# Optimization experiments

Hardware: AMD Instinct MI355X
Metric: run time of the kernel (lower is better)

The kernel has to match this reference:

```python
import jax, jax.numpy as jnp
import numpy as np

NUM_NODES = 100000
NUM_EDGES = 1200000
IN_CH = 64
HID_CH = 64
NUM_REL = 8
DEG = NUM_EDGES // NUM_NODES  # uniform degree 12


def setup_inputs() -> dict:
    key = jax.random.key(0)
    k1, k2, k3, k4 = jax.random.split(key, 4)
    x = jax.random.normal(k1, (NUM_NODES, IN_CH), dtype=jnp.float32)
    linear = jax.random.normal(k2, (NUM_REL, IN_CH, HID_CH), dtype=jnp.float32) * (1.0 / np.sqrt(IN_CH))
    ptr = jnp.arange(NUM_NODES + 1, dtype=jnp.int64) * DEG  # CSR row pointers, uniform degree
    idx = jax.random.randint(k3, (NUM_EDGES,), 0, NUM_NODES, dtype=jnp.int64)
    edge_types = jax.random.randint(k4, (NUM_EDGES,), 0, NUM_REL, dtype=jnp.int64)
    return {"x": x, "linear": linear, "ptr": ptr, "idx": idx,
            "edge_types": edge_types, "num_node": NUM_NODES}


def reference(x, linear, ptr, idx, edge_types, num_node):
    # Gather source-node features per edge: [E, in]
    gathered = x[idx]
    # Per-edge-type linear transform (loop over small fixed num_rel, like RGCNOP)
    out_e = jnp.zeros((gathered.shape[0], linear.shape[-1]), dtype=gathered.dtype)
    for r in range(linear.shape[0]):
        mask = (edge_types == r).astype(gathered.dtype)[:, None]
        out_e = out_e + mask * (gathered @ linear[r])
    # CSR scatter-sum aggregation over destination segments defined by ptr
    num_edges = idx.shape[0]
    seg_ids = jnp.searchsorted(ptr, jnp.arange(num_edges, dtype=ptr.dtype), side='right') - 1
    agg = jax.ops.segment_sum(out_e, seg_ids, num_segments=num_node)
    # Degree normalization
    deg = (ptr[1:] - ptr[:-1]).astype(agg.dtype)
    return agg / deg[:, None]
```

## Files before the change

kernel.cpp:

```cpp
#include <hip/hip_runtime.h>
#include <hip/hip_bf16.h>
#include <hip/hip_fp16.h>


#define THREADS 512
#define NPB 32
#define KDIM 512
#define LDA 520
#define MAXE 512
#define WFRAG (4 * 16 * 64 * 8)

typedef __attribute__((ext_vector_type(8))) short bf16x8;
typedef __attribute__((ext_vector_type(4))) float f32x4;
typedef __attribute__((ext_vector_type(8))) unsigned short u16x8;

extern __shared__ __align__(16) char smem[];

__device__ __forceinline__ unsigned short f2bf(float f) {
  __hip_bfloat16 h = __float2bfloat16(f);
  return *reinterpret_cast<unsigned short*>(&h);
}

__device__ __forceinline__ float h2f(unsigned short u) {
  __half h;
  *reinterpret_cast<unsigned short*>(&h) = u;
  return __half2float(h);
}

__global__ __launch_bounds__(256) void pack_w(const void* __restrict__ wv,
                                              unsigned short* __restrict__ wsB) {
  const int lane = threadIdx.x & 63;
  const unsigned word = ((const unsigned*)wv)[lane];
  const int exf = (int)((word >> 7) & 0xFFu);
  const bool w_bf16 = __popcll(__ballot(exf >= 96 && exf < 160)) >= 48;
  for (int i = blockIdx.x * 256 + threadIdx.x; i < WFRAG; i += gridDim.x * 256) {
    const int j  = i & 7;
    const int l  = (i >> 3) & 63;
    const int kt = (i >> 9) & 15;
    const int nt = i >> 13;
    const int k  = kt * 32 + (l >> 4) * 8 + j;
    const int n  = nt * 16 + (l & 15);
    float v;
    if (w_bf16) v = __bfloat162float(((const __hip_bfloat16*)wv)[k * 64 + n]);
    else        v = ((const float*)wv)[k * 64 + n];
    wsB[i] = f2bf(v);
  }
}

__global__ __launch_bounds__(256) void pack_x(const void* __restrict__ xv,
                                              unsigned short* __restrict__ wsX,
                                              int total8) {
  const int lane = threadIdx.x & 63;
  const unsigned word = ((const unsigned*)xv)[lane];
  const int exf = (int)((word >> 7) & 0xFFu);
  const bool x_bf16 = __popcll(__ballot(exf >= 96 && exf < 160)) >= 48;
  if (x_bf16) return;
  const f32x4* xf = (const f32x4*)xv;
  for (int i = blockIdx.x * 256 + threadIdx.x; i < total8; i += gridDim.x * 256) {
    const f32x4 a = xf[i * 2 + 0];
    const f32x4 b = xf[i * 2 + 1];
    u16x8 o;
    __half h;
    h = __float2half(a[0]); o[0] = *reinterpret_cast<unsigned short*>(&h);
    h = __float2half(a[1]); o[1] = *reinterpret_cast<unsigned short*>(&h);
    h = __float2half(a[2]); o[2] = *reinterpret_cast<unsigned short*>(&h);
    h = __float2half(a[3]); o[3] = *reinterpret_cast<unsigned short*>(&h);
    h = __float2half(b[0]); o[4] = *reinterpret_cast<unsigned short*>(&h);
    h = __float2half(b[1]); o[5] = *reinterpret_cast<unsigned short*>(&h);
    h = __float2half(b[2]); o[6] = *reinterpret_cast<unsigned short*>(&h);
    h = __float2half(b[3]); o[7] = *reinterpret_cast<unsigned short*>(&h);
    ((u16x8*)wsX)[i] = o;
  }
}

#define ACC_SW(accrow, r, vv)                                        \
  switch (r) {                                                       \
    case 0: accrow[0] += (vv); break; case 1: accrow[1] += (vv); break; \
    case 2: accrow[2] += (vv); break; case 3: accrow[3] += (vv); break; \
    case 4: accrow[4] += (vv); break; case 5: accrow[5] += (vv); break; \
    case 6: accrow[6] += (vv); break; default: accrow[7] += (vv); break; }

__global__ __launch_bounds__(THREADS, 6)
void rgcn_fused(const void* __restrict__ xv,
                const void* __restrict__ wv,
                const int* __restrict__ p32,
                const int* __restrict__ i32,
                const int* __restrict__ t32,
                const unsigned short* __restrict__ wsB,
                const unsigned short* __restrict__ wsX,
                float* __restrict__ out,
                int num_nodes) {
  __hip_bfloat16* aggS = (__hip_bfloat16*)smem;
  __hip_bfloat16* wtS  = aggS + (NPB + 1) * LDA;
  char* tail = smem + (size_t)(NPB + 1) * LDA * 2 +
               (wsB ? 0 : (size_t)64 * LDA * 2);
  float*    invS  = (float*)tail;
  int*      ptrS  = (int*)(tail + 256);
  unsigned* eMeta = (unsigned*)(tail + 256 + 144);

  const int tid   = threadIdx.x;
  const int lane  = tid & 63;
  const int wvid  = tid >> 6;
  const int node0 = blockIdx.x * NPB;

  const unsigned xword = ((const unsigned*)xv)[lane];
  const int exf = (int)((xword >> 7) & 0xFFu);
  const bool x_bf16 = __popcll(__ballot(exf >= 96 && exf < 160)) >= 48;
  const bool idx64 = (p32[1] == 0);

  auto ldptr = [&](int n) -> int { return idx64 ? p32[2 * n] : p32[n]; };

  const int ntop   = min(node0 + NPB, num_nodes);
  const int e_lo   = ldptr(node0);
  const int ecount = ldptr(ntop) - e_lo;
  const bool staged = (ecount > 0 && ecount <= MAXE);

  for (int i = tid; i <= NPB; i += THREADS)
    ptrS[i] = ldptr(min(node0 + i, num_nodes));

  if (staged) {
    for (int e = tid; e < ecount; e += THREADS) {
      const int ge = e_lo + e;
      const unsigned s = (unsigned)(idx64 ? i32[2 * ge] : i32[ge]);
      const unsigned r = (unsigned)(idx64 ? t32[2 * ge] : t32[ge]);
      eMeta[e] = s | (r << 24);
    }
  }

  if (!wsB) {
    if (x_bf16) {
      const __hip_bfloat16* wb = (const __hip_bfloat16*)wv;
      for (int i = tid; i < KDIM * 64; i += THREADS)
        wtS[(i & 63) * LDA + (i >> 6)] = wb[i];
    } else {
      const float* wf = (const float*)wv;
      for (int i = tid; i < KDIM * 64; i += THREADS)
        wtS[(i & 63) * LDA + (i >> 6)] = __float2bfloat16(wf[i]);
    }
  }

  __syncthreads();

  for (int i = tid; i < NPB; i += THREADS) {
    const int d = ptrS[i + 1] - ptrS[i];
    invS[i] = (d > 0 && node0 + i < num_nodes) ? 1.0f / (float)d : 0.0f;
  }

  if (staged) {
    for (int n = tid; n < NPB; n += THREADS) {
      const int b0 = ptrS[n] - e_lo;
      const int d  = ptrS[n + 1] - ptrS[n];
      if (d == 12) {
        unsigned mm[12];
        unsigned long long cnt = 0;
#pragma unroll
        for (int i = 0; i < 12; ++i) {
          mm[i] = eMeta[b0 + i];
          cnt += 1ull << ((mm[i] >> 24) * 4);
        }
        unsigned long long off = 0;
        unsigned run = 0;
#pragma unroll
        for (int r = 0; r < 8; ++r) {
          off |= (unsigned long long)run << (r * 4);
          run += (unsigned)((cnt >> (r * 4)) & 15ull);
        }
#pragma unroll
        for (int i = 0; i < 12; ++i) {
          const int sh = (int)(mm[i] >> 24) * 4;
          const unsigned slot = (unsigned)((off >> sh) & 15ull);
          off += 1ull << sh;
          eMeta[b0 + (int)slot] = mm[i];
        }
      }
    }
  }

  {
    f32x4* z = (f32x4*)aggS;
    const f32x4 zero = {0.f, 0.f, 0.f, 0.f};
    const int nvec = (NPB + 1) * LDA * 2 / 16;
    for (int i = tid; i < nvec; i += THREADS) z[i] = zero;
  }

  __syncthreads();

  const int c16 = lane & 15;
  const int qd  = lane >> 4;

  auto gather = [&](auto xp, auto loadrow) {
    const int nlb = wvid * 4;
    const int eq0 = ptrS[nlb + qd] - e_lo;
    const int dq  = ptrS[nlb + qd + 1] - e_lo - eq0;
    const bool okfast = staged && (node0 + nlb + 3 < num_nodes) &&
                        (__ballot(dq == 12) == ~0ull);
    if (okfast) {
      unsigned m[12];
      unsigned rr[12];
#pragma unroll
      for (int j = 0; j < 12; ++j) m[j] = eMeta[eq0 + j];
#pragma unroll
      for (int j = 0; j < 12; ++j) rr[j] = m[j] >> 24;
      f32x4 v[12];
#pragma unroll
      for (int j = 0; j < 12; ++j)
        v[j] = loadrow((int)(m[j] & 0x00FFFFFFu), c16);
      unsigned short* nodeP =
          (unsigned short*)(aggS + (size_t)(nlb + qd) * LDA) + 4 * c16;
      unsigned short* dumpP =
          (unsigned short*)(aggS + (size_t)NPB * LDA) + qd * 136 + 4 * c16;
      f32x4 A = {0.f, 0.f, 0.f, 0.f};
#pragma unroll
      for (int j = 0; j < 12; ++j) {
        A += v[j];
        const bool b = (j == 11) || (rr[j] != rr[j + 1 < 12 ? j + 1 : 11]);
        ushort4 bb;
        bb.x = f2bf(A[0]); bb.y = f2bf(A[1]);
        bb.z = f2bf(A[2]); bb.w = f2bf(A[3]);
        unsigned short* dst = b ? (nodeP + (rr[j] << 6)) : dumpP;
        *(ushort4*)dst = bb;
        A = b ? (f32x4){0.f, 0.f, 0.f, 0.f} : A;
      }
    } else {
#pragma unroll
      for (int t = 0; t < 4; ++t) {
        const int nl = nlb + t;
        float a[8] = {0.f, 0.f, 0.f, 0.f, 0.f, 0.f, 0.f, 0.f};
        if (node0 + nl < num_nodes) {
          const int e0 = ptrS[nl] - e_lo, e1 = ptrS[nl + 1] - e_lo;
          for (int e = e0; e < e1; ++e) {
            unsigned mm;
            if (staged) mm = eMeta[e];
            else {
              const int ge = e_lo + e;
              mm = (unsigned)(idx64 ? i32[2 * ge] : i32[ge]) |
                   ((unsigned)(idx64 ? t32[2 * ge] : t32[ge]) << 24);
            }
            const float vv = xp((size_t)(mm & 0x00FFFFFFu) * 64 + lane);
            const int r = __builtin_amdgcn_readfirstlane((int)(mm >> 24));
            ACC_SW(a, r, vv)
          }
        }
#pragma unroll
        for (int r = 0; r < 8; ++r)
          aggS[(size_t)nl * LDA + r * 64 + lane] = __float2bfloat16(a[r]);
      }
    }
  };

  if (!x_bf16 && wsX) {
    auto xp = [&](size_t i) -> float { return h2f(wsX[i]); };
    auto lr = [&](int src, int c) -> f32x4 {
      const ushort4 u = ((const ushort4*)wsX)[(size_t)src * 16 + c];
      f32x4 f;
      f[0] = h2f(u.x); f[1] = h2f(u.y); f[2] = h2f(u.z); f[3] = h2f(u.w);
      return f;
    };
    gather(xp, lr);
  } else if (x_bf16) {
    auto xp = [&](size_t i) -> float {
      const unsigned short u = ((const unsigned short*)xv)[i];
      return __uint_as_float((unsigned)u << 16);
    };
    auto lr = [&](int src, int c) -> f32x4 {
      const ushort4 u = ((const ushort4*)xv)[(size_t)src * 16 + c];
      f32x4 f;
      f[0] = __uint_as_float((unsigned)(unsigned short)u.x << 16);
      f[1] = __uint_as_float((unsigned)(unsigned short)u.y << 16);
      f[2] = __uint_as_float((unsigned)(unsigned short)u.z << 16);
      f[3] = __uint_as_float((unsigned)(unsigned short)u.w << 16);
      return f;
    };
    gather(xp, lr);
  } else {
    auto xp = [&](size_t i) -> float { return ((const float*)xv)[i]; };
    auto lr = [&](int src, int c) -> f32x4 {
      return ((const f32x4*)xv)[(size_t)src * 16 + c];
    };
    gather(xp, lr);
  }

  __syncthreads();

  const int mt = wvid >> 2;
  const int nt = wvid & 3;
  const int mi = lane & 15;
  const int q4 = lane >> 4;
  const __hip_bfloat16* ap = aggS + (size_t)(mt * 16 + mi) * LDA + q4 * 8;
  f32x4 c0 = {0.f, 0.f, 0.f, 0.f};
  if (wsB) {
    const bf16x8* B = (const bf16x8*)wsB;
#pragma unroll
    for (int kt = 0; kt < KDIM / 32; ++kt) {
      const bf16x8 a = *(const bf16x8*)(ap + kt * 32);
      const bf16x8 b = B[(nt * 16 + kt) * 64 + lane];
      c0 = __builtin_amdgcn_mfma_f32_16x16x32_bf16(a, b, c0, 0, 0, 0);
    }
  } else {
    const __hip_bfloat16* bp = wtS + (size_t)(nt * 16 + mi) * LDA + q4 * 8;
#pragma unroll
    for (int kt = 0; kt < KDIM / 32; ++kt) {
      const bf16x8 a = *(const bf16x8*)(ap + kt * 32);
      const bf16x8 b = *(const bf16x8*)(bp + kt * 32);
      c0 = __builtin_amdgcn_mfma_f32_16x16x32_bf16(a, b, c0, 0, 0, 0);
    }
  }

#pragma unroll
  for (int i = 0; i < 4; ++i) {
    const int row  = q4 * 4 + i;
    const int nl   = mt * 16 + row;
    const int node = node0 + nl;
    if (node < num_nodes) {
      out[(size_t)node * 64 + nt * 16 + mi] = c0[i] * invS[nl];
    }
  }
}

extern "C" void kernel_launch(void* const* d_in, const int* in_sizes, int n_in,
                              void* d_out, int out_size, void* d_ws, size_t ws_size,
                              hipStream_t stream) {
  const void* x   = d_in[0];
  const void* w   = d_in[1];
  const int*  ptr = (const int*)d_in[2];
  const int*  idx = (const int*)d_in[3];
  const int*  et  = (const int*)d_in[4];
  float*      out = (float*)d_out;

  const int num_nodes = in_sizes[0] / 64;

  const size_t needW = (size_t)WFRAG * sizeof(unsigned short);
  const size_t needX = needW + (size_t)num_nodes * 64 * 2;
  const bool useWs = (d_ws != nullptr) && (ws_size >= needW);
  const bool useX  = (d_ws != nullptr) && (ws_size >= needX);
  unsigned short* wsB = useWs ? (unsigned short*)d_ws : nullptr;
  unsigned short* wsX = useX ? (unsigned short*)((char*)d_ws + needW) : nullptr;

  if (useWs) pack_w<<<32, 256, 0, stream>>>(w, wsB);
  if (useX)  pack_x<<<1024, 256, 0, stream>>>(x, wsX, num_nodes * 8);

  const size_t lds_bytes = (size_t)(NPB + 1) * LDA * 2 +
                           (useWs ? 0 : (size_t)64 * LDA * 2) +
                           256 + 144 + (size_t)MAXE * 4;

  hipFuncSetAttribute((const void*)rgcn_fused,
                      hipFuncAttributeMaxDynamicSharedMemorySize,
                      (int)lds_bytes);

  const int nblocks = (num_nodes + NPB - 1) / NPB;
  rgcn_fused<<<nblocks, THREADS, lds_bytes, stream>>>(x, w, ptr, idx, et, wsB,
                                                      wsX, out, num_nodes);
}
```

Measured before the change: 127.8 us.

## Merge pack kernels and prepack edge metadata into workspace

Combines the weight and x packing kernels into one launch that also packs each edge's source index and relation type into a single 32-bit word in the workspace. The main kernel then reads one word per edge instead of two int64 arrays, which cuts its index traffic. Output stores become nontemporal. In exchange the pre-pass must read and write all edge metadata every call, which adds a full extra pass over the index arrays.

```diff
diff --git a/kernel.cpp b/kernel.cpp
--- a/kernel.cpp
+++ b/kernel.cpp
@@ -27,49 +27,66 @@
   return __half2float(h);
 }
 
-__global__ __launch_bounds__(256) void pack_w(const void* __restrict__ wv,
-                                              unsigned short* __restrict__ wsB) {
+__global__ __launch_bounds__(256)
+void pack_all(const void* __restrict__ xv, const void* __restrict__ wv,
+              const int* __restrict__ p32, const int* __restrict__ i32,
+              const int* __restrict__ t32,
+              unsigned short* __restrict__ wsB,
+              unsigned* __restrict__ wsM,
+              unsigned short* __restrict__ wsX,
+              int num_nodes, int idx_words) {
   const int lane = threadIdx.x & 63;
-  const unsigned word = ((const unsigned*)wv)[lane];
-  const int exf = (int)((word >> 7) & 0xFFu);
-  const bool w_bf16 = __popcll(__ballot(exf >= 96 && exf < 160)) >= 48;
-  for (int i = blockIdx.x * 256 + threadIdx.x; i < WFRAG; i += gridDim.x * 256) {
-    const int j  = i & 7;
-    const int l  = (i >> 3) & 63;
-    const int kt = (i >> 9) & 15;
-    const int nt = i >> 13;
-    const int k  = kt * 32 + (l >> 4) * 8 + j;
-    const int n  = nt * 16 + (l & 15);
-    float v;
-    if (w_bf16) v = __bfloat162float(((const __hip_bfloat16*)wv)[k * 64 + n]);
-    else        v = ((const float*)wv)[k * 64 + n];
-    wsB[i] = f2bf(v);
-  }
-}
-
-__global__ __launch_bounds__(256) void pack_x(const void* __restrict__ xv,
-                                              unsigned short* __restrict__ wsX,
-                                              int total8) {
-  const int lane = threadIdx.x & 63;
-  const unsigned word = ((const unsigned*)xv)[lane];
-  const int exf = (int)((word >> 7) & 0xFFu);
-  const bool x_bf16 = __popcll(__ballot(exf >= 96 && exf < 160)) >= 48;
-  if (x_bf16) return;
-  const f32x4* xf = (const f32x4*)xv;
-  for (int i = blockIdx.x * 256 + threadIdx.x; i < total8; i += gridDim.x * 256) {
-    const f32x4 a = xf[i * 2 + 0];
-    const f32x4 b = xf[i * 2 + 1];
-    u16x8 o;
-    __half h;
-    h = __float2half(a[0]); o[0] = *reinterpret_cast<unsigned short*>(&h);
-    h = __float2half(a[1]); o[1] = *reinterpret_cast<unsigned short*>(&h);
-    h = __float2half(a[2]); o[2] = *reinterpret_cast<unsigned short*>(&h);
-    h = __float2half(a[3]); o[3] = *reinterpret_cast<unsigned short*>(&h);
-    h = __float2half(b[0]); o[4] = *reinterpret_cast<unsigned short*>(&h);
-    h = __float2half(b[1]); o[5] = *reinterpret_cast<unsigned short*>(&h);
-    h = __float2half(b[2]); o[6] = *reinterpret_cast<unsigned short*>(&h);
-    h = __float2half(b[3]); o[7] = *reinterpret_cast<unsigned short*>(&h);
-    ((u16x8*)wsX)[i] = o;
+  const unsigned wword = ((const unsigned*)wv)[lane];
+  const int exw = (int)((wword >> 7) & 0xFFu);
+  const bool w_bf16 = __popcll(__ballot(exw >= 96 && exw < 160)) >= 48;
+  const unsigned xword = ((const unsigned*)xv)[lane];
+  const int exx = (int)((xword >> 7) & 0xFFu);
+  const bool x_bf16 = __popcll(__ballot(exx >= 96 && exx < 160)) >= 48;
+  const bool idx64 = (p32[1] == 0);
+
+  const int gs = gridDim.x * 256;
+  const int g0 = blockIdx.x * 256 + threadIdx.x;
+
+  if (wsB) {
+    for (int i = g0; i < WFRAG; i += gs) {
+      const int j  = i & 7;
+      const int l  = (i >> 3) & 63;
+      const int kt = (i >> 9) & 15;
+      const int nt = i >> 13;
+      const int k  = kt * 32 + (l >> 4) * 8 + j;
+      const int n  = nt * 16 + (l & 15);
+      float v;
+      if (w_bf16) v = __bfloat162float(((const __hip_bfloat16*)wv)[k * 64 + n]);
+      else        v = ((const float*)wv)[k * 64 + n];
+      wsB[i] = f2bf(v);
+    }
+  }
+  if (wsM) {
+    const int E = idx64 ? (idx_words >> 1) : idx_words;
+    for (int e = g0; e < E; e += gs) {
+      const unsigned s = (unsigned)(idx64 ? i32[2 * e] : i32[e]);
+      const unsigned r = (unsigned)(idx64 ? t32[2 * e] : t32[e]);
+      wsM[e] = s | (r << 24);
+    }
+  }
+  if (wsX && !x_bf16) {
+    const f32x4* xf = (const f32x4*)xv;
+    const int total8 = num_nodes * 8;
+    for (int i = g0; i < total8; i += gs) {
+      const f32x4 a = xf[i * 2 + 0];
+      const f32x4 b = xf[i * 2 + 1];
+      u16x8 o;
+      __half h;
+      h = __float2half(a[0]); o[0] = *reinterpret_cast<unsigned short*>(&h);
+      h = __float2half(a[1]); o[1] = *reinterpret_cast<unsigned short*>(&h);
+      h = __float2half(a[2]); o[2] = *reinterpret_cast<unsigned short*>(&h);
+      h = __float2half(a[3]); o[3] = *reinterpret_cast<unsigned short*>(&h);
+      h = __float2half(b[0]); o[4] = *reinterpret_cast<unsigned short*>(&h);
+      h = __float2half(b[1]); o[5] = *reinterpret_cast<unsigned short*>(&h);
+      h = __float2half(b[2]); o[6] = *reinterpret_cast<unsigned short*>(&h);
+      h = __float2half(b[3]); o[7] = *reinterpret_cast<unsigned short*>(&h);
+      ((u16x8*)wsX)[i] = o;
+    }
   }
 }
 
@@ -87,6 +104,7 @@
                 const int* __restrict__ i32,
                 const int* __restrict__ t32,
                 const unsigned short* __restrict__ wsB,
+                const unsigned* __restrict__ wsM,
                 const unsigned short* __restrict__ wsX,
                 float* __restrict__ out,
                 int num_nodes) {
@@ -119,11 +137,16 @@
     ptrS[i] = ldptr(min(node0 + i, num_nodes));
 
   if (staged) {
-    for (int e = tid; e < ecount; e += THREADS) {
-      const int ge = e_lo + e;
-      const unsigned s = (unsigned)(idx64 ? i32[2 * ge] : i32[ge]);
-      const unsigned r = (unsigned)(idx64 ? t32[2 * ge] : t32[ge]);
-      eMeta[e] = s | (r << 24);
+    if (wsM) {
+      for (int e = tid; e < ecount; e += THREADS)
+        eMeta[e] = __builtin_nontemporal_load(wsM + e_lo + e);
+    } else {
+      for (int e = tid; e < ecount; e += THREADS) {
+        const int ge = e_lo + e;
+        const unsigned s = (unsigned)(idx64 ? i32[2 * ge] : i32[ge]);
+        const unsigned r = (unsigned)(idx64 ? t32[2 * ge] : t32[ge]);
+        eMeta[e] = s | (r << 24);
+      }
     }
   }
 
@@ -231,6 +254,7 @@
           for (int e = e0; e < e1; ++e) {
             unsigned mm;
             if (staged) mm = eMeta[e];
+            else if (wsM) mm = wsM[e_lo + e];
             else {
               const int ge = e_lo + e;
               mm = (unsigned)(idx64 ? i32[2 * ge] : i32[ge]) |
@@ -312,7 +336,8 @@
     const int nl   = mt * 16 + row;
     const int node = node0 + nl;
     if (node < num_nodes) {
-      out[(size_t)node * 64 + nt * 16 + mi] = c0[i] * invS[nl];
+      const float v = c0[i] * invS[nl];
+      __builtin_nontemporal_store(v, &out[(size_t)node * 64 + nt * 16 + mi]);
     }
   }
 }
@@ -328,16 +353,24 @@
   float*      out = (float*)d_out;
 
   const int num_nodes = in_sizes[0] / 64;
+  const int idx_words = in_sizes[3];
 
   const size_t needW = (size_t)WFRAG * sizeof(unsigned short);
-  const size_t needX = needW + (size_t)num_nodes * 64 * 2;
+  const size_t offM  = (needW + 15) & ~(size_t)15;
+  const size_t needM = offM + (size_t)idx_words * 4;
+  const size_t offX  = (needM + 15) & ~(size_t)15;
+  const size_t needX = offX + (size_t)num_nodes * 64 * 2;
+
   const bool useWs = (d_ws != nullptr) && (ws_size >= needW);
+  const bool useM  = (d_ws != nullptr) && (ws_size >= needM);
   const bool useX  = (d_ws != nullptr) && (ws_size >= needX);
   unsigned short* wsB = useWs ? (unsigned short*)d_ws : nullptr;
-  unsigned short* wsX = useX ? (unsigned short*)((char*)d_ws + needW) : nullptr;
-
-  if (useWs) pack_w<<<32, 256, 0, stream>>>(w, wsB);
-  if (useX)  pack_x<<<1024, 256, 0, stream>>>(x, wsX, num_nodes * 8);
+  unsigned*       wsM = useM ? (unsigned*)((char*)d_ws + offM) : nullptr;
+  unsigned short* wsX = useX ? (unsigned short*)((char*)d_ws + offX) : nullptr;
+
+  if (useWs)
+    pack_all<<<2048, 256, 0, stream>>>(x, w, ptr, idx, et, wsB, wsM, wsX,
+                                       num_nodes, idx_words);
 
   const size_t lds_bytes = (size_t)(NPB + 1) * LDA * 2 +
                            (useWs ? 0 : (size_t)64 * LDA * 2) +
@@ -349,5 +382,5 @@
 
   const int nblocks = (num_nodes + NPB - 1) / NPB;
   rgcn_fused<<<nblocks, THREADS, lds_bytes, stream>>>(x, w, ptr, idx, et, wsB,
-                                                      wsX, out, num_nodes);
-}
+                                                      wsM, wsX, out, num_nodes);
+}
```

New measurement: 125.7 us, median of 2. Within noise of the previous version (-1.7%).
